# Kernel tuning notes

Measured on AMD Instinct MI355X. Metric: run time of the kernel, lower is better.

## Reference

```python
import jax, jax.numpy as jnp
import numpy as np

N = 100000      # nodes (dtype==2 subgraph)
E = 1600000     # edges
IN_DIM = 256
OUT_DIM = 64
FEAT_DIM = 64   # hard-coded by nn.Linear(64, out_dim) in dstfeat_fc


def setup_inputs() -> dict:
    key = jax.random.key(0)
    k1, k2, k3, k4, k5, k6 = jax.random.split(key, 6)
    h = jax.random.normal(k1, (N, IN_DIM), dtype=jnp.float32)
    feat = jax.random.normal(k2, (N, FEAT_DIM), dtype=jnp.float32)
    W_fc = jax.random.normal(k3, (OUT_DIM, IN_DIM), dtype=jnp.float32) * 0.05
    W_dst = jax.random.normal(k4, (OUT_DIM, FEAT_DIM), dtype=jnp.float32) * 0.05
    src = jax.random.randint(k5, (E,), 0, N, dtype=jnp.int64)
    dst = jax.random.randint(k6, (E,), 0, N, dtype=jnp.int64)
    return {"h": h, "feat": feat, "W_fc": W_fc, "W_dst": W_dst, "src": src, "dst": dst}


def reference(h, feat, W_fc, W_dst, src, dst):
    # node projections (done once per node, then gathered per edge)
    z = h @ W_fc.T            # [N, OUT]  (self.fc)
    df = feat @ W_dst.T       # [N, OUT]  (self.dstfeat_fc on dst 'feat')

    # per-edge attention logit: dot(z[src], dstfeat[dst])
    e = jnp.sum(z[src] * df[dst], axis=-1)          # [E]

    # segment softmax over incoming edges of each destination node
    emax = jax.ops.segment_max(e, dst, num_segments=N)
    emax = jnp.where(jnp.isfinite(emax), emax, 0.0)  # guard empty segments
    ex = jnp.exp(e - emax[dst])                      # [E]
    denom = jax.ops.segment_sum(ex, dst, num_segments=N)  # [N]

    # weighted neighbor aggregation: sum_e alpha_e * z[src_e] per dst
    num = jax.ops.segment_sum(ex[:, None] * z[src], dst, num_segments=N)  # [N, OUT]
    out = num / jnp.where(denom == 0, 1.0, denom)[:, None]
    return out
```

## Files before the change

### kernel.cpp

```cpp
#include <hip/hip_runtime.h>
#include <math.h>

typedef unsigned int uint32;
typedef __attribute__((ext_vector_type(8))) short bf16x8;
typedef __attribute__((ext_vector_type(4))) float f32x4;

__device__ __forceinline__ ushort f2bf(float f) {
  uint32 u = __builtin_bit_cast(uint32, f);
  uint32 r = (u + 0x7fff + ((u >> 16) & 1)) >> 16;
  return (ushort)r;
}
__device__ __forceinline__ float bf_lo(uint32 u) {
  return __builtin_bit_cast(float, u << 16);
}
__device__ __forceinline__ float bf_hi(uint32 u) {
  return __builtin_bit_cast(float, u & 0xffff0000u);
}

template <int K, bool BF16OUT>
__device__ __forceinline__ void gemm_body(const float* __restrict__ A,
                                          const float* __restrict__ W,
                                          ushort* __restrict__ Cb,
                                          float* __restrict__ C,
                                          int M, int bx, ushort* Ws) {
  const int t = threadIdx.x;
  const int lane = t & 63;
  const int w = t >> 6;
  const int quad = lane >> 4;
  const int l16 = lane & 15;
  const int rBase = bx * 128;
  const int WSTR = K + 8;

  const int kq4 = K >> 2;
  for (int idx = t; idx < 64 * kq4; idx += 256) {
    int row = idx / kq4, kq = idx - row * kq4;
    float4 v = *(const float4*)(W + (size_t)row * K + kq * 4);
    ushort4 b;
    b.x = f2bf(v.x); b.y = f2bf(v.y); b.z = f2bf(v.z); b.w = f2bf(v.w);
    *(ushort4*)&Ws[row * WSTR + kq * 4] = b;
  }
  __syncthreads();

  f32x4 acc[2][4];
  #pragma unroll
  for (int i = 0; i < 2; ++i)
    #pragma unroll
    for (int n = 0; n < 4; ++n) acc[i][n] = (f32x4){0.f, 0.f, 0.f, 0.f};

  const int r0 = min(rBase + w * 32 + l16, M - 1);
  const int r1 = min(rBase + w * 32 + 16 + l16, M - 1);
  const float* __restrict__ a0 = A + (size_t)r0 * K + quad * 8;
  const float* __restrict__ a1 = A + (size_t)r1 * K + quad * 8;

  #pragma unroll 2
  for (int kb = 0; kb < K; kb += 32) {
    float4 v00 = *(const float4*)(a0 + kb);
    float4 v01 = *(const float4*)(a0 + kb + 4);
    float4 v10 = *(const float4*)(a1 + kb);
    float4 v11 = *(const float4*)(a1 + kb + 4);
    bf16x8 af0, af1;
    af0[0] = (short)f2bf(v00.x); af0[1] = (short)f2bf(v00.y);
    af0[2] = (short)f2bf(v00.z); af0[3] = (short)f2bf(v00.w);
    af0[4] = (short)f2bf(v01.x); af0[5] = (short)f2bf(v01.y);
    af0[6] = (short)f2bf(v01.z); af0[7] = (short)f2bf(v01.w);
    af1[0] = (short)f2bf(v10.x); af1[1] = (short)f2bf(v10.y);
    af1[2] = (short)f2bf(v10.z); af1[3] = (short)f2bf(v10.w);
    af1[4] = (short)f2bf(v11.x); af1[5] = (short)f2bf(v11.y);
    af1[6] = (short)f2bf(v11.z); af1[7] = (short)f2bf(v11.w);

    bf16x8 bfrag[4];
    #pragma unroll
    for (int n = 0; n < 4; ++n)
      bfrag[n] = *(const bf16x8*)&Ws[(n * 16 + l16) * WSTR + kb + quad * 8];

    #pragma unroll
    for (int n = 0; n < 4; ++n) {
      acc[0][n] = __builtin_amdgcn_mfma_f32_16x16x32_bf16(af0, bfrag[n], acc[0][n], 0, 0, 0);
      acc[1][n] = __builtin_amdgcn_mfma_f32_16x16x32_bf16(af1, bfrag[n], acc[1][n], 0, 0, 0);
    }
  }

  #pragma unroll
  for (int i = 0; i < 2; ++i)
    #pragma unroll
    for (int nt = 0; nt < 4; ++nt)
      #pragma unroll
      for (int r = 0; r < 4; ++r) {
        int row = rBase + w * 32 + i * 16 + quad * 4 + r;
        int col = nt * 16 + l16;
        if (row < M) {
          if (BF16OUT)
            Cb[(size_t)row * 64 + col] = f2bf(acc[i][nt][r]);
          else
            C[(size_t)row * 64 + col] = acc[i][nt][r];
        }
      }
}

__global__ __launch_bounds__(256, 4) void gemm_both(const float* __restrict__ h,
                                                    const float* __restrict__ feat,
                                                    const float* __restrict__ W_fc,
                                                    const float* __restrict__ W_dst,
                                                    ushort* __restrict__ zb,
                                                    float* __restrict__ df,
                                                    int M, int gsplit) {
  __shared__ __align__(16) ushort Ws[64 * 264];
  if ((int)blockIdx.x < gsplit)
    gemm_body<256, true>(h, W_fc, zb, nullptr, M, (int)blockIdx.x, Ws);
  else
    gemm_body<64, false>(feat, W_dst, nullptr, df, M, (int)blockIdx.x - gsplit, Ws);
}

#define NBBITS 9
#define BKNODES 512
#define CH 4096
#define NBMAX 256

__global__ __launch_bounds__(256) void csr_count(const int* __restrict__ dst,
                                                 int* __restrict__ bCnt, int E, int NB) {
  __shared__ int lcnt[NBMAX];
  const int t = threadIdx.x;
  if (t < NB) lcnt[t] = 0;
  __syncthreads();
  const int c0 = blockIdx.x * CH, c1 = min(c0 + CH, E);
  for (int i = c0 + t; i < c1; i += 256) atomicAdd(&lcnt[dst[i] >> NBBITS], 1);
  __syncthreads();
  if (t < NB) {
    int c = lcnt[t];
    if (c) atomicAdd(&bCnt[t], c);
  }
}

__global__ __launch_bounds__(256) void csr_scan(const int* __restrict__ bCnt,
                                                int* __restrict__ bBase,
                                                int* __restrict__ bCursor,
                                                int* __restrict__ offsets,
                                                int NB, int N, int E) {
  __shared__ int wsum[4];
  const int t = threadIdx.x;
  const int lane = t & 63, wave = t >> 6;
  int x = (t < NB) ? bCnt[t] : 0;
  int inc = x;
  #pragma unroll
  for (int d = 1; d < 64; d <<= 1) {
    int o = __shfl_up(inc, d, 64);
    if (lane >= d) inc += o;
  }
  if (lane == 63) wsum[wave] = inc;
  __syncthreads();
  int wbase = 0;
  #pragma unroll
  for (int w = 0; w < 4; ++w)
    if (w < wave) wbase += wsum[w];
  int excl = wbase + inc - x;
  if (t < NB) {
    bBase[t] = excl;
    bCursor[t] = excl;
  }
  if (t == 0) {
    bBase[NB] = E;
    offsets[N] = E;
  }
}

__global__ __launch_bounds__(256) void csr_partition(const int* __restrict__ src,
                                                     const int* __restrict__ dst,
                                                     int* __restrict__ bCursor,
                                                     unsigned* __restrict__ packed,
                                                     int E, int NB) {
  __shared__ int lcnt[NBMAX];
  __shared__ int lbase[NBMAX];
  const int t = threadIdx.x;
  if (t < NB) lcnt[t] = 0;
  __syncthreads();
  const int c0 = blockIdx.x * CH, c1 = min(c0 + CH, E);
  for (int i = c0 + t; i < c1; i += 256) atomicAdd(&lcnt[dst[i] >> NBBITS], 1);
  __syncthreads();
  if (t < NB) {
    int c = lcnt[t];
    lbase[t] = c ? atomicAdd(&bCursor[t], c) : 0;
  }
  __syncthreads();
  for (int i = c0 + t; i < c1; i += 256) {
    int dv = dst[i];
    int b = dv >> NBBITS;
    int pos = atomicAdd(&lbase[b], 1);
    packed[pos] = ((unsigned)src[i] << NBBITS) | (unsigned)(dv & (BKNODES - 1));
  }
}

__global__ __launch_bounds__(256) void csr_finalize(const int* __restrict__ bBase,
                                                    const unsigned* __restrict__ packed,
                                                    int* __restrict__ edgeSrc,
                                                    int* __restrict__ offsets, int N) {
  __shared__ int sh[BKNODES];
  __shared__ int wsum[4];
  const int r = blockIdx.x;
  const int t = threadIdx.x;
  const int lane = t & 63, wave = t >> 6;
  const int base = bBase[r];
  const int endr = bBase[r + 1];
  for (int i = t; i < BKNODES; i += 256) sh[i] = 0;
  __syncthreads();
  for (int i = base + t; i < endr; i += 256)
    atomicAdd(&sh[packed[i] & (BKNODES - 1)], 1);
  __syncthreads();
  {
    int cA = sh[2 * t], cB = sh[2 * t + 1];
    int s = cA + cB;
    int inc = s;
    #pragma unroll
    for (int d = 1; d < 64; d <<= 1) {
      int o = __shfl_up(inc, d, 64);
      if (lane >= d) inc += o;
    }
    if (lane == 63) wsum[wave] = inc;
    __syncthreads();
    int wbase = 0;
    #pragma unroll
    for (int w = 0; w < 4; ++w)
      if (w < wave) wbase += wsum[w];
    int excl = wbase + inc - s;
    sh[2 * t] = base + excl;
    sh[2 * t + 1] = base + excl + cA;
  }
  __syncthreads();
  const int node0 = r << NBBITS;
  for (int k = t; k < BKNODES; k += 256) {
    int g = node0 + k;
    if (g < N) offsets[g] = sh[k];
  }
  __syncthreads();
  for (int i = base + t; i < endr; i += 256) {
    unsigned v = packed[i];
    int pos = atomicAdd(&sh[v & (BKNODES - 1)], 1);
    edgeSrc[pos] = (int)(v >> NBBITS);
  }
}

__global__ __launch_bounds__(256) void aggregate(const ushort* __restrict__ zb,
                                                 const float* __restrict__ df,
                                                 const int* __restrict__ offsets,
                                                 const int* __restrict__ edgeSrc,
                                                 float* __restrict__ out, int N) {
  int gwave = (blockIdx.x * blockDim.x + threadIdx.x) >> 6;
  int lane = threadIdx.x & 63;
  if (gwave >= N) return;
  const int d = __builtin_amdgcn_readfirstlane(gwave);
  const int g = lane >> 4;
  const int l16 = lane & 15;
  const int beg = offsets[d];
  const int end = offsets[d + 1];

  const float4 df4 = *(const float4*)(df + (size_t)d * 64 + l16 * 4);

  float m = -INFINITY, l = 0.f;
  float ax = 0.f, ay = 0.f, az = 0.f, aw = 0.f;

  for (int j0 = beg; j0 < end; j0 += 32) {
    const int nst = min(8, (end - j0 + 3) >> 2);
    uint2 zf[8];
    float ew[8];
    float bm = -INFINITY;

    #pragma unroll
    for (int st = 0; st < 8; ++st) {
      if (st < nst) {
        const int eidx = j0 + st * 4 + g;
        const bool act = eidx < end;
        int s = 0;
        if (act) s = edgeSrc[eidx];
        zf[st] = *(const uint2*)(zb + (size_t)s * 64 + l16 * 4);
        float p = bf_lo(zf[st].x) * df4.x;
        p = fmaf(bf_hi(zf[st].x), df4.y, p);
        p = fmaf(bf_lo(zf[st].y), df4.z, p);
        p = fmaf(bf_hi(zf[st].y), df4.w, p);
        p += __shfl_xor(p, 1, 64);
        p += __shfl_xor(p, 2, 64);
        p += __shfl_xor(p, 4, 64);
        p += __shfl_xor(p, 8, 64);
        ew[st] = act ? p : -INFINITY;
        bm = fmaxf(bm, ew[st]);
      }
    }
    bm = fmaxf(bm, __shfl_xor(bm, 16, 64));
    bm = fmaxf(bm, __shfl_xor(bm, 32, 64));

    const float nm = fmaxf(m, bm);
    const float alpha = __expf(m - nm);
    float sw = 0.f;
    #pragma unroll
    for (int st = 0; st < 8; ++st) {
      if (st < nst) {
        const float w = __expf(ew[st] - nm);
        ew[st] = w;
        sw += w;
      }
    }
    sw += __shfl_xor(sw, 16, 64);
    sw += __shfl_xor(sw, 32, 64);
    l = l * alpha + sw;
    m = nm;

    ax *= alpha; ay *= alpha; az *= alpha; aw *= alpha;
    #pragma unroll
    for (int st = 0; st < 8; ++st) {
      if (st < nst) {
        const float w = ew[st];
        ax = fmaf(w, bf_lo(zf[st].x), ax);
        ay = fmaf(w, bf_hi(zf[st].x), ay);
        az = fmaf(w, bf_lo(zf[st].y), az);
        aw = fmaf(w, bf_hi(zf[st].y), aw);
      }
    }
  }

  ax += __shfl_xor(ax, 16, 64); ax += __shfl_xor(ax, 32, 64);
  ay += __shfl_xor(ay, 16, 64); ay += __shfl_xor(ay, 32, 64);
  az += __shfl_xor(az, 16, 64); az += __shfl_xor(az, 32, 64);
  aw += __shfl_xor(aw, 16, 64); aw += __shfl_xor(aw, 32, 64);

  if (lane < 16) {
    const float inv = (l > 0.f) ? (1.f / l) : 0.f;
    float4 o;
    o.x = ax * inv; o.y = ay * inv; o.z = az * inv; o.w = aw * inv;
    *(float4*)(out + (size_t)d * 64 + l16 * 4) = o;
  }
}

extern "C" void kernel_launch(void* const* d_in, const int* in_sizes, int n_in,
                              void* d_out, int out_size, void* d_ws, size_t ws_size,
                              hipStream_t stream) {
  const float* h     = (const float*)d_in[0];
  const float* feat  = (const float*)d_in[1];
  const float* W_fc  = (const float*)d_in[2];
  const float* W_dst = (const float*)d_in[3];
  const int*   src   = (const int*)d_in[4];
  const int*   dst   = (const int*)d_in[5];
  float* out = (float*)d_out;

  const int N = in_sizes[1] / 64;
  const int E = in_sizes[4];

  const int NB = (N + BKNODES - 1) >> NBBITS;
  const int nChunks = (E + CH - 1) / CH;

  char* ws = (char*)d_ws;
  ushort* zb = (ushort*)ws;
  float* df = (float*)(zb + (size_t)N * 64);
  int* offsets = (int*)(df + (size_t)N * 64);
  int* edgeSrc = offsets + N + 1;
  int* bCnt = edgeSrc + E;
  int* bBase = bCnt + NB;
  int* bCursor = bBase + NB + 1;
  unsigned* packed = (unsigned*)d_out;

  hipMemsetAsync(bCnt, 0, sizeof(int) * (size_t)NB, stream);

  const int gsplit = (N + 127) / 128;
  gemm_both<<<gsplit * 2, 256, 0, stream>>>(h, feat, W_fc, W_dst, zb, df, N, gsplit);

  csr_count<<<nChunks, 256, 0, stream>>>(dst, bCnt, E, NB);
  csr_scan<<<1, 256, 0, stream>>>(bCnt, bBase, bCursor, offsets, NB, N, E);
  csr_partition<<<nChunks, 256, 0, stream>>>(src, dst, bCursor, packed, E, NB);
  csr_finalize<<<NB, 256, 0, stream>>>(bBase, packed, edgeSrc, offsets, N);

  aggregate<<<(N + 3) / 4, 256, 0, stream>>>(zb, df, offsets, edgeSrc, out, N);
}
```

Before: 350.9 us.

## Shrink CSR buckets to 256 nodes and make aggregate a persistent grid-stride kernel

Halves the CSR bucket size so there are about twice as many buckets (up to 512). csr_finalize now runs one node per thread and the scan kernel grows to 512 threads. The aggregate kernel becomes persistent with 2048 blocks; each wave walks destination nodes in grid-stride order and prefetches the next node's offsets and df row while it processes the current one. The goal is more parallelism in finalize and less launch and wave-startup overhead in aggregate, at the cost of more global atomics in count/partition and possible load imbalance across the fixed wave count.

```diff
diff --git a/kernel.cpp b/kernel.cpp
--- a/kernel.cpp
+++ b/kernel.cpp
@@ -111,32 +111,32 @@
     gemm_body<64, false>(feat, W_dst, nullptr, df, M, (int)blockIdx.x - gsplit, Ws);
 }
 
-#define NBBITS 9
-#define BKNODES 512
+#define NBBITS 8
+#define BKNODES 256
 #define CH 4096
-#define NBMAX 256
+#define NBMAX 512
 
 __global__ __launch_bounds__(256) void csr_count(const int* __restrict__ dst,
                                                  int* __restrict__ bCnt, int E, int NB) {
   __shared__ int lcnt[NBMAX];
   const int t = threadIdx.x;
-  if (t < NB) lcnt[t] = 0;
+  for (int i = t; i < NB; i += 256) lcnt[i] = 0;
   __syncthreads();
   const int c0 = blockIdx.x * CH, c1 = min(c0 + CH, E);
   for (int i = c0 + t; i < c1; i += 256) atomicAdd(&lcnt[dst[i] >> NBBITS], 1);
   __syncthreads();
-  if (t < NB) {
-    int c = lcnt[t];
-    if (c) atomicAdd(&bCnt[t], c);
-  }
-}
-
-__global__ __launch_bounds__(256) void csr_scan(const int* __restrict__ bCnt,
+  for (int b = t; b < NB; b += 256) {
+    int c = lcnt[b];
+    if (c) atomicAdd(&bCnt[b], c);
+  }
+}
+
+__global__ __launch_bounds__(512) void csr_scan(const int* __restrict__ bCnt,
                                                 int* __restrict__ bBase,
                                                 int* __restrict__ bCursor,
                                                 int* __restrict__ offsets,
                                                 int NB, int N, int E) {
-  __shared__ int wsum[4];
+  __shared__ int wsum[8];
   const int t = threadIdx.x;
   const int lane = t & 63, wave = t >> 6;
   int x = (t < NB) ? bCnt[t] : 0;
@@ -150,7 +150,7 @@
   __syncthreads();
   int wbase = 0;
   #pragma unroll
-  for (int w = 0; w < 4; ++w)
+  for (int w = 0; w < 8; ++w)
     if (w < wave) wbase += wsum[w];
   int excl = wbase + inc - x;
   if (t < NB) {
@@ -171,14 +171,14 @@
   __shared__ int lcnt[NBMAX];
   __shared__ int lbase[NBMAX];
   const int t = threadIdx.x;
-  if (t < NB) lcnt[t] = 0;
+  for (int i = t; i < NB; i += 256) lcnt[i] = 0;
   __syncthreads();
   const int c0 = blockIdx.x * CH, c1 = min(c0 + CH, E);
   for (int i = c0 + t; i < c1; i += 256) atomicAdd(&lcnt[dst[i] >> NBBITS], 1);
   __syncthreads();
-  if (t < NB) {
-    int c = lcnt[t];
-    lbase[t] = c ? atomicAdd(&bCursor[t], c) : 0;
+  for (int b = t; b < NB; b += 256) {
+    int c = lcnt[b];
+    lbase[b] = c ? atomicAdd(&bCursor[b], c) : 0;
   }
   __syncthreads();
   for (int i = c0 + t; i < c1; i += 256) {
@@ -200,15 +200,14 @@
   const int lane = t & 63, wave = t >> 6;
   const int base = bBase[r];
   const int endr = bBase[r + 1];
-  for (int i = t; i < BKNODES; i += 256) sh[i] = 0;
+  sh[t] = 0;
   __syncthreads();
   for (int i = base + t; i < endr; i += 256)
     atomicAdd(&sh[packed[i] & (BKNODES - 1)], 1);
   __syncthreads();
   {
-    int cA = sh[2 * t], cB = sh[2 * t + 1];
-    int s = cA + cB;
-    int inc = s;
+    int x = sh[t];
+    int inc = x;
     #pragma unroll
     for (int d = 1; d < 64; d <<= 1) {
       int o = __shfl_up(inc, d, 64);
@@ -220,15 +219,15 @@
     #pragma unroll
     for (int w = 0; w < 4; ++w)
       if (w < wave) wbase += wsum[w];
-    int excl = wbase + inc - s;
-    sh[2 * t] = base + excl;
-    sh[2 * t + 1] = base + excl + cA;
+    int excl = wbase + inc - x;
+    __syncthreads();
+    sh[t] = base + excl;
   }
   __syncthreads();
   const int node0 = r << NBBITS;
-  for (int k = t; k < BKNODES; k += 256) {
-    int g = node0 + k;
-    if (g < N) offsets[g] = sh[k];
+  {
+    int g = node0 + t;
+    if (g < N) offsets[g] = sh[t];
   }
   __syncthreads();
   for (int i = base + t; i < endr; i += 256) {
@@ -242,89 +241,99 @@
                                                  const float* __restrict__ df,
                                                  const int* __restrict__ offsets,
                                                  const int* __restrict__ edgeSrc,
-                                                 float* __restrict__ out, int N) {
-  int gwave = (blockIdx.x * blockDim.x + threadIdx.x) >> 6;
-  int lane = threadIdx.x & 63;
-  if (gwave >= N) return;
-  const int d = __builtin_amdgcn_readfirstlane(gwave);
+                                                 float* __restrict__ out, int N, int NW) {
+  const int lane = threadIdx.x & 63;
+  int d = __builtin_amdgcn_readfirstlane((int)((blockIdx.x * blockDim.x + threadIdx.x) >> 6));
+  if (d >= N) return;
   const int g = lane >> 4;
   const int l16 = lane & 15;
-  const int beg = offsets[d];
-  const int end = offsets[d + 1];
-
-  const float4 df4 = *(const float4*)(df + (size_t)d * 64 + l16 * 4);
-
-  float m = -INFINITY, l = 0.f;
-  float ax = 0.f, ay = 0.f, az = 0.f, aw = 0.f;
-
-  for (int j0 = beg; j0 < end; j0 += 32) {
-    const int nst = min(8, (end - j0 + 3) >> 2);
-    uint2 zf[8];
-    float ew[8];
-    float bm = -INFINITY;
-
-    #pragma unroll
-    for (int st = 0; st < 8; ++st) {
-      if (st < nst) {
-        const int eidx = j0 + st * 4 + g;
-        const bool act = eidx < end;
-        int s = 0;
-        if (act) s = edgeSrc[eidx];
-        zf[st] = *(const uint2*)(zb + (size_t)s * 64 + l16 * 4);
-        float p = bf_lo(zf[st].x) * df4.x;
-        p = fmaf(bf_hi(zf[st].x), df4.y, p);
-        p = fmaf(bf_lo(zf[st].y), df4.z, p);
-        p = fmaf(bf_hi(zf[st].y), df4.w, p);
-        p += __shfl_xor(p, 1, 64);
-        p += __shfl_xor(p, 2, 64);
-        p += __shfl_xor(p, 4, 64);
-        p += __shfl_xor(p, 8, 64);
-        ew[st] = act ? p : -INFINITY;
-        bm = fmaxf(bm, ew[st]);
+
+  int beg = offsets[d];
+  int end = offsets[d + 1];
+  float4 df4 = *(const float4*)(df + (size_t)d * 64 + l16 * 4);
+
+  while (true) {
+    const int nd = d + NW;
+    const int ndc = min(nd, N - 1);
+    const int nbeg = offsets[ndc];
+    const int nend = offsets[ndc + 1];
+    const float4 ndf4 = *(const float4*)(df + (size_t)ndc * 64 + l16 * 4);
+
+    float m = -INFINITY, l = 0.f;
+    float ax = 0.f, ay = 0.f, az = 0.f, aw = 0.f;
+
+    for (int j0 = beg; j0 < end; j0 += 32) {
+      const int nst = min(8, (end - j0 + 3) >> 2);
+      uint2 zf[8];
+      float ew[8];
+      float bm = -INFINITY;
+
+      #pragma unroll
+      for (int st = 0; st < 8; ++st) {
+        if (st < nst) {
+          const int eidx = j0 + st * 4 + g;
+          const bool act = eidx < end;
+          int s = 0;
+          if (act) s = edgeSrc[eidx];
+          zf[st] = *(const uint2*)(zb + (size_t)s * 64 + l16 * 4);
+          float p = bf_lo(zf[st].x) * df4.x;
+          p = fmaf(bf_hi(zf[st].x), df4.y, p);
+          p = fmaf(bf_lo(zf[st].y), df4.z, p);
+          p = fmaf(bf_hi(zf[st].y), df4.w, p);
+          p += __shfl_xor(p, 1, 64);
+          p += __shfl_xor(p, 2, 64);
+          p += __shfl_xor(p, 4, 64);
+          p += __shfl_xor(p, 8, 64);
+          ew[st] = act ? p : -INFINITY;
+          bm = fmaxf(bm, ew[st]);
+        }
+      }
+      bm = fmaxf(bm, __shfl_xor(bm, 16, 64));
+      bm = fmaxf(bm, __shfl_xor(bm, 32, 64));
+
+      const float nm = fmaxf(m, bm);
+      const float alpha = __expf(m - nm);
+      float sw = 0.f;
+      #pragma unroll
+      for (int st = 0; st < 8; ++st) {
+        if (st < nst) {
+          const float w = __expf(ew[st] - nm);
+          ew[st] = w;
+          sw += w;
+        }
+      }
+      sw += __shfl_xor(sw, 16, 64);
+      sw += __shfl_xor(sw, 32, 64);
+      l = l * alpha + sw;
+      m = nm;
+
+      ax *= alpha; ay *= alpha; az *= alpha; aw *= alpha;
+      #pragma unroll
+      for (int st = 0; st < 8; ++st) {
+        if (st < nst) {
+          const float w = ew[st];
+          ax = fmaf(w, bf_lo(zf[st].x), ax);
+          ay = fmaf(w, bf_hi(zf[st].x), ay);
+          az = fmaf(w, bf_lo(zf[st].y), az);
+          aw = fmaf(w, bf_hi(zf[st].y), aw);
+        }
       }
     }
-    bm = fmaxf(bm, __shfl_xor(bm, 16, 64));
-    bm = fmaxf(bm, __shfl_xor(bm, 32, 64));
-
-    const float nm = fmaxf(m, bm);
-    const float alpha = __expf(m - nm);
-    float sw = 0.f;
-    #pragma unroll
-    for (int st = 0; st < 8; ++st) {
-      if (st < nst) {
-        const float w = __expf(ew[st] - nm);
-        ew[st] = w;
-        sw += w;
-      }
+
+    ax += __shfl_xor(ax, 16, 64); ax += __shfl_xor(ax, 32, 64);
+    ay += __shfl_xor(ay, 16, 64); ay += __shfl_xor(ay, 32, 64);
+    az += __shfl_xor(az, 16, 64); az += __shfl_xor(az, 32, 64);
+    aw += __shfl_xor(aw, 16, 64); aw += __shfl_xor(aw, 32, 64);
+
+    if (lane < 16) {
+      const float inv = (l > 0.f) ? (1.f / l) : 0.f;
+      float4 o;
+      o.x = ax * inv; o.y = ay * inv; o.z = az * inv; o.w = aw * inv;
+      *(float4*)(out + (size_t)d * 64 + l16 * 4) = o;
     }
-    sw += __shfl_xor(sw, 16, 64);
-    sw += __shfl_xor(sw, 32, 64);
-    l = l * alpha + sw;
-    m = nm;
-
-    ax *= alpha; ay *= alpha; az *= alpha; aw *= alpha;
-    #pragma unroll
-    for (int st = 0; st < 8; ++st) {
-      if (st < nst) {
-        const float w = ew[st];
-        ax = fmaf(w, bf_lo(zf[st].x), ax);
-        ay = fmaf(w, bf_hi(zf[st].x), ay);
-        az = fmaf(w, bf_lo(zf[st].y), az);
-        aw = fmaf(w, bf_hi(zf[st].y), aw);
-      }
-    }
-  }
-
-  ax += __shfl_xor(ax, 16, 64); ax += __shfl_xor(ax, 32, 64);
-  ay += __shfl_xor(ay, 16, 64); ay += __shfl_xor(ay, 32, 64);
-  az += __shfl_xor(az, 16, 64); az += __shfl_xor(az, 32, 64);
-  aw += __shfl_xor(aw, 16, 64); aw += __shfl_xor(aw, 32, 64);
-
-  if (lane < 16) {
-    const float inv = (l > 0.f) ? (1.f / l) : 0.f;
-    float4 o;
-    o.x = ax * inv; o.y = ay * inv; o.z = az * inv; o.w = aw * inv;
-    *(float4*)(out + (size_t)d * 64 + l16 * 4) = o;
+
+    if (nd >= N) break;
+    d = nd; beg = nbeg; end = nend; df4 = ndf4;
   }
 }
 
@@ -361,9 +370,11 @@
   gemm_both<<<gsplit * 2, 256, 0, stream>>>(h, feat, W_fc, W_dst, zb, df, N, gsplit);
 
   csr_count<<<nChunks, 256, 0, stream>>>(dst, bCnt, E, NB);
-  csr_scan<<<1, 256, 0, stream>>>(bCnt, bBase, bCursor, offsets, NB, N, E);
+  csr_scan<<<1, 512, 0, stream>>>(bCnt, bBase, bCursor, offsets, NB, N, E);
   csr_partition<<<nChunks, 256, 0, stream>>>(src, dst, bCursor, packed, E, NB);
   csr_finalize<<<NB, 256, 0, stream>>>(bBase, packed, edgeSrc, offsets, N);
 
-  aggregate<<<(N + 3) / 4, 256, 0, stream>>>(zb, df, offsets, edgeSrc, out, N);
-}
+  const int aggBlocks = 2048;
+  const int NW = aggBlocks * 4;
+  aggregate<<<aggBlocks, 256, 0, stream>>>(zb, df, offsets, edgeSrc, out, N, NW);
+}
```

After: 335.2 us. 4.5% less time.
